# Kernel optimization log

Measured on AMD Instinct MI355X. Metric: run time of the kernel, lower is better.

The kernel has to match this reference:

```python
import jax, jax.numpy as jnp
import numpy as np
from jax.scipy.special import i0

# torchkbnufft default configuration
N = 256          # image size per dim (im_size)
OSF = 2          # grid oversampling factor (default grid_size = 2*im_size)
G = N * OSF      # oversampled grid size = 512
W = 6            # kernel width (numpoints default)
ALPHA = 2.34 * W # Kaiser-Bessel shape parameter (kbwidth default 2.34)
M = 65536        # number of non-uniform k-space samples
B, C = 2, 8      # batch, coils


def _kb_ft(t):
    """Analytic Fourier transform of the KB kernel (for deapodization)."""
    s2 = ALPHA ** 2 - (jnp.pi * W * t) ** 2
    z = jnp.sqrt(jnp.abs(s2)) + 1e-12
    return jnp.where(s2 >= 0, jnp.sinh(z) / z, jnp.sin(z) / z)


def _kb(d):
    """Kaiser-Bessel interpolation kernel, d = distance in grid units."""
    u = 1.0 - (2.0 * d / W) ** 2
    return jnp.where(u > 0, i0(ALPHA * jnp.sqrt(jnp.maximum(u, 1e-12))), 0.0) / W


def setup_inputs() -> dict:
    key = jax.random.key(0)
    k1, k2 = jax.random.split(key)
    x_image = jax.random.normal(k1, (B, C, N, N), dtype=jnp.float32)
    # trajectory in radians/sample, uniform in [-pi, pi)
    k_traj = (jax.random.uniform(k2, (2, M), dtype=jnp.float32) - 0.5) * (2 * jnp.pi)
    return {"x_image": x_image, "k_traj": k_traj}


def reference(x_image, k_traj):
    # 1) deapodization (scaling coefficients), centered image convention
    n = jnp.arange(N, dtype=jnp.float32) - N / 2
    sc = 1.0 / _kb_ft(n / G)                       # (N,)
    xs = (x_image * (sc[:, None] * sc[None, :])).astype(jnp.complex64)

    # 2) zero-pad onto oversampled grid with image centered at index 0 (mod G)
    grid = jnp.zeros(x_image.shape[:2] + (G, G), jnp.complex64)
    grid = grid.at[..., :N, :N].set(xs)
    grid = jnp.roll(grid, shift=(-(N // 2), -(N // 2)), axis=(-2, -1))
    Xk = jnp.fft.fft2(grid)                        # (B,C,G,G) uniform k-space

    # 3) KB interpolation onto non-uniform points (irregular gather)
    tm = k_traj * (G / (2 * jnp.pi))               # continuous grid coords, (2,M)
    offs = jnp.arange(-(W // 2) + 1, W // 2 + 1, dtype=jnp.float32)  # [-2..3]
    base = jnp.floor(tm)
    pts = base[:, :, None] + offs                  # (2,M,W) neighbor coords
    wts = _kb(tm[:, :, None] - pts)                # (2,M,W) real weights
    idx = pts.astype(jnp.int32) % G                # wrap (periodic grid)

    gathered = Xk[:, :, idx[0][:, :, None], idx[1][:, None, :]]  # (B,C,M,W,W)
    y = jnp.einsum('bcmij,mi,mj->bcm', gathered,
                   wts[0].astype(jnp.complex64), wts[1].astype(jnp.complex64))
    # return complex result as stacked (real, imag) float32 for the harness
    return jnp.stack([y.real, y.imag], axis=-1)   # (B,C,M,2)
```

## Files before the change

kernel.cpp:

```cpp
#include <hip/hip_runtime.h>
#include <hip/hip_fp16.h>
#include <math.h>

#define NN 256
#define GSZ 512
#define GG (GSZ * GSZ)
#define BC 16
#define MM 65536
#define ALPHA_C 14.04f
#define WKER 6
#define PI_F 3.14159265358979f
#define RC2 0.70710678118654752f
#define KSCALE 81.48733086305042f

#define SSCALE 16777216.0f
#define INV_SSCALE 5.9604644775390625e-8f

#define CAP 160
#define TRW 21
#define TPITCH 23
#define PLANE (TRW * TPITCH)
#define QPL 4
#define NPQ (QPL * TRW * TRW)

__device__ __forceinline__ __half2* gh_plane(float2* grid, int bc) {
    return (__half2*)((char*)grid + (size_t)bc * (GG * 8) + 524288);
}
__device__ __forceinline__ const __half2* gh_plane_c(const float2* grid, int bc) {
    return (const __half2*)((const char*)grid + (size_t)bc * (GG * 8) + 524288);
}


__device__ __forceinline__ float bessel_i0(float x) {
    if (x < 3.75f) {
        float t = x * (1.0f / 3.75f);
        float t2 = t * t;
        return 1.0f + t2 * (3.5156229f + t2 * (3.0899424f + t2 * (1.2067492f +
                     t2 * (0.2659732f + t2 * (0.0360768f + t2 * 0.0045813f)))));
    } else {
        float t = 3.75f / x;
        float p = 0.39894228f + t * (0.01328592f + t * (0.00225319f + t * (-0.00157565f +
                  t * (0.00916281f + t * (-0.02057706f + t * (0.02635537f +
                  t * (-0.01647633f + t * 0.00392377f)))))));
        return p * __expf(x) * rsqrtf(x);
    }
}

__device__ __forceinline__ float kb_weight(float d) {
    float r = d * (2.0f / (float)WKER);
    float u = 1.0f - r * r;
    if (u <= 0.0f) return 0.0f;
    return bessel_i0(ALPHA_C * sqrtf(u)) * (1.0f / (float)WKER);
}

__device__ __forceinline__ float kb_ft_inv(float t) {
    float a = PI_F * (float)WKER * t;
    float s2 = ALPHA_C * ALPHA_C - a * a;
    float z = sqrtf(fabsf(s2)) + 1e-12f;
    float sh = 0.5f * (__expf(z) - __expf(-z));
    return z / sh;
}

__device__ __forceinline__ void cmul(float& zr, float& zi, float wr, float wi) {
    float r = zr * wr - zi * wi;
    zi = zr * wi + zi * wr;
    zr = r;
}


template <int L>
__device__ __forceinline__ void radix8_stage(float* pr, float* pi_, int j) {
    int pos = j & (L - 1);
    int base = (j - pos) * 8 + pos;
    float ar[8], ai[8];
#pragma unroll
    for (int r = 0; r < 8; ++r) {
        int idx = base + r * L;
        int ph = idx + (idx >> 3);
        ar[r] = pr[ph];
        ai[r] = pi_[ph];
    }
    if (L > 1) {
        float th = (float)pos * (-PI_F / (4.0f * (float)L));
        float s1, c1;
        __sincosf(th, &s1, &c1);
        float wr = c1, wi = s1;
#pragma unroll
        for (int r = 1; r < 8; ++r) {
            cmul(ar[r], ai[r], wr, wi);
            float nr = wr * c1 - wi * s1;
            wi = wr * s1 + wi * c1;
            wr = nr;
        }
    }
    float s0r = ar[0] + ar[4], s0i = ai[0] + ai[4];
    float d0r = ar[0] - ar[4], d0i = ai[0] - ai[4];
    float s1r = ar[2] + ar[6], s1i = ai[2] + ai[6];
    float d1r = ar[2] - ar[6], d1i = ai[2] - ai[6];
    float E0r = s0r + s1r, E0i = s0i + s1i;
    float E2r = s0r - s1r, E2i = s0i - s1i;
    float E1r = d0r + d1i, E1i = d0i - d1r;
    float E3r = d0r - d1i, E3i = d0i + d1r;
    float u0r = ar[1] + ar[5], u0i = ai[1] + ai[5];
    float v0r = ar[1] - ar[5], v0i = ai[1] - ai[5];
    float u1r = ar[3] + ar[7], u1i = ai[3] + ai[7];
    float v1r = ar[3] - ar[7], v1i = ai[3] - ai[7];
    float O0r = u0r + u1r, O0i = u0i + u1i;
    float O2r = u0r - u1r, O2i = u0i - u1i;
    float O1r = v0r + v1i, O1i = v0i - v1r;
    float O3r = v0r - v1i, O3i = v0i + v1r;
    float t1r = RC2 * (O1r + O1i), t1i = RC2 * (O1i - O1r);
    float t2r = O2i,               t2i = -O2r;
    float t3r = RC2 * (O3i - O3r), t3i = -RC2 * (O3r + O3i);
    float xr[8], xi[8];
    xr[0] = E0r + O0r; xi[0] = E0i + O0i;
    xr[4] = E0r - O0r; xi[4] = E0i - O0i;
    xr[1] = E1r + t1r; xi[1] = E1i + t1i;
    xr[5] = E1r - t1r; xi[5] = E1i - t1i;
    xr[2] = E2r + t2r; xi[2] = E2i + t2i;
    xr[6] = E2r - t2r; xi[6] = E2i - t2i;
    xr[3] = E3r + t3r; xi[3] = E3i + t3i;
    xr[7] = E3r - t3r; xi[7] = E3i - t3i;
#pragma unroll
    for (int q = 0; q < 8; ++q) {
        int idx = base + q * L;
        int ph = idx + (idx >> 3);
        pr[ph] = xr[q];
        pi_[ph] = xi[q];
    }
}


#define LDSP 576
__global__ void __launch_bounds__(256) k_fft_row(const float* __restrict__ x,
                                                 float2* __restrict__ grid) {
    __shared__ float re[4][LDSP], im[4][LDSP];
    int b = blockIdx.x;
    int t = threadIdx.x;
    int w = t >> 6;
    int l = t & 63;
    int rg = (b & 63) * 4 + w;
    int bc = b >> 6;
    int r = (rg < 128) ? rg : rg + 256;
    int r_img = rg ^ 128;
    float scx = kb_ft_inv((float)(r_img - 128) * (1.0f / (float)GSZ));
    const float* xrow = x + ((size_t)bc * NN + (size_t)r_img) * NN;
#pragma unroll
    for (int e = 0; e < 8; ++e) {
        int i = e * 64 + l;
        float v = 0.0f;
        if (i < 128 || i >= 384) {
            int y = (i + 128) & (GSZ - 1);
            float scy = kb_ft_inv((float)(y - 128) * (1.0f / (float)GSZ));
            v = xrow[y] * scx * scy;
        }
        int rev = (l & 7) * 64 + (l >> 3) * 8 + e;
        int ph = rev + (rev >> 3);
        re[w][ph] = v;
        im[w][ph] = 0.0f;
    }
    __syncthreads();
    radix8_stage<1>(re[w], im[w], l);
    __syncthreads();
    radix8_stage<8>(re[w], im[w], l);
    __syncthreads();
    radix8_stage<64>(re[w], im[w], l);
    __syncthreads();
    size_t gbase = (size_t)bc * GG + (size_t)r * GSZ;
#pragma unroll
    for (int e = 0; e < 8; ++e) {
        int k = e * 64 + l;
        int ph = k + (k >> 3);
        grid[gbase + k] = make_float2(re[w][ph], im[w][ph]);
    }
}

#define CSTR 577
__global__ void __launch_bounds__(256) k_fft_col(float2* __restrict__ grid) {
    __shared__ float re[16][CSTR], im[16][CSTR];
    int b = blockIdx.x;
    int bc = b >> 5;
    int c0 = (b & 31) << 4;
    size_t base = (size_t)bc * GG + (size_t)c0;
    int t = threadIdx.x;
#pragma unroll
    for (int it = 0; it < 32; ++it) {
        int idx = it * 256 + t;
        int row = idx >> 4, col = idx & 15;
        float2 v = make_float2(0.0f, 0.0f);
        if (row < 128 || row >= 384)
            v = grid[base + (size_t)row * GSZ + col];
        int rev = (row & 7) * 64 + ((row >> 3) & 7) * 8 + (row >> 6);
        int ph = rev + (rev >> 3);
        re[col][ph] = v.x;
        im[col][ph] = v.y;
    }
    __syncthreads();
    int col = t & 15, jg = t >> 4;
#pragma unroll
    for (int k = 0; k < 4; ++k) radix8_stage<1>(re[col], im[col], jg + 16 * k);
    __syncthreads();
#pragma unroll
    for (int k = 0; k < 4; ++k) radix8_stage<8>(re[col], im[col], jg + 16 * k);
    __syncthreads();
#pragma unroll
    for (int k = 0; k < 4; ++k) radix8_stage<64>(re[col], im[col], jg + 16 * k);
    __syncthreads();
    __half2* ghp = gh_plane(grid, bc);
#pragma unroll
    for (int it = 0; it < 32; ++it) {
        int idx = it * 256 + t;
        int row = idx >> 4, c = idx & 15;
        int ph = row + (row >> 3);
        ghp[(size_t)row * GSZ + c0 + c] = __float22half2_rn(
            make_float2(re[c][ph] * SSCALE, im[c][ph] * SSCALE));
    }
}


__global__ void k_bin(const float* __restrict__ kt, unsigned* __restrict__ cnt,
                      unsigned short* __restrict__ ubuf) {
    int m = blockIdx.x * blockDim.x + threadIdx.x;
    float tmx = kt[m] * KSCALE;
    float tmy = kt[MM + m] * KSCALE;
    int ibx = (int)floorf(tmx) & (GSZ - 1);
    int iby = (int)floorf(tmy) & (GSZ - 1);
    int tile = ((ibx >> 4) << 5) | (iby >> 4);
    unsigned slot = atomicAdd(&cnt[tile], 1u);
    if (slot < CAP) ubuf[(size_t)tile * CAP + slot] = (unsigned short)m;
}


__global__ void __launch_bounds__(128) k_gather_tile(
    const float2* __restrict__ grid, const float* __restrict__ kt,
    const unsigned* __restrict__ cnt, const unsigned short* __restrict__ ubuf,
    float2* __restrict__ out) {
    __shared__ __half2 ldsh[QPL * PLANE];
    __shared__ float wts[CAP][13];
    __shared__ unsigned lxy[CAP];
    int bid = blockIdx.x;
    int b = ((bid & 7) << 9) | (bid >> 3);
    int tile = b >> 2;
    int quad = b & 3;
    int bc0 = quad * QPL;
    int tx0 = (tile >> 5) << 4;
    int ty0 = (tile & 31) << 4;
    int t = threadIdx.x;
#pragma unroll
    for (int k = 0; k < 14; ++k) {
        int idx = t + (k << 7);
        if (idx < NPQ) {
            int p = idx / (TRW * TRW);
            int rem = idx - p * (TRW * TRW);
            int r = rem / TRW;
            int c = rem - r * TRW;
            int row = (tx0 - 2 + r) & (GSZ - 1);
            int col = (ty0 - 2 + c) & (GSZ - 1);
            ldsh[p * PLANE + r * TPITCH + c] =
                gh_plane_c(grid, bc0 + p)[(size_t)row * GSZ + col];
        }
    }
    int n = (int)cnt[tile];
    if (n > CAP) n = CAP;
    for (int p = t; p < n; p += 128) {
        int m = (int)ubuf[(size_t)tile * CAP + p];
        float tmx = kt[m] * KSCALE;
        float tmy = kt[MM + m] * KSCALE;
        float bx = floorf(tmx), by = floorf(tmy);
#pragma unroll
        for (int o = 0; o < 6; ++o) {
            float offv = (float)(o - 2);
            wts[p][o]     = kb_weight(tmx - (bx + offv)) * INV_SSCALE;
            wts[p][6 + o] = kb_weight(tmy - (by + offv));
        }
        int lx = (int)bx & 15;
        int ly = (int)by & 15;
        lxy[p] = ((unsigned)m << 8) | (unsigned)(lx << 4) | (unsigned)ly;
    }
    __syncthreads();
    int g = t >> 6;
    int baseA = (2 * g) * PLANE;
    int baseB = baseA + PLANE;
    int bcA = bc0 + 2 * g, bcB = bcA + 1;
    for (int s = (t & 63); s < n; s += 64) {
        unsigned lc = lxy[s];
        int m = (int)(lc >> 8);
        int lx = (int)((lc >> 4) & 15u);
        int ly = (int)(lc & 15u);
        float w0v[6], w1v[6];
#pragma unroll
        for (int o = 0; o < 6; ++o) {
            w0v[o] = wts[s][o];
            w1v[o] = wts[s][6 + o];
        }
        int off0 = lx * TPITCH + ly;
        float arA = 0.f, aiA = 0.f, arB = 0.f, aiB = 0.f;
#pragma unroll
        for (int ii = 0; ii < 6; ++ii) {
            float wi = w0v[ii];
            int rowoff = off0 + ii * TPITCH;
#pragma unroll
            for (int j = 0; j < 6; ++j) {
                float wv = wi * w1v[j];
                int o = rowoff + j;
                float2 vA = __half22float2(ldsh[baseA + o]);
                float2 vB = __half22float2(ldsh[baseB + o]);
                arA = fmaf(wv, vA.x, arA);
                aiA = fmaf(wv, vA.y, aiA);
                arB = fmaf(wv, vB.x, arB);
                aiB = fmaf(wv, vB.y, aiB);
            }
        }
        out[(size_t)bcA * MM + m] = make_float2(arA, aiA);
        out[(size_t)bcB * MM + m] = make_float2(arB, aiB);
    }
}

__global__ void k_gather(const float2* __restrict__ grid, const float* __restrict__ kt,
                         float2* __restrict__ out) {
    int tid = blockIdx.x * blockDim.x + threadIdx.x;
    int m = tid & (MM - 1);
    int bc = tid >> 16;
    float tmx = kt[m] * KSCALE;
    float tmy = kt[MM + m] * KSCALE;
    float bx = floorf(tmx), by = floorf(tmy);
    int ibx = (int)bx, iby = (int)by;
    float w0[6], w1[6];
    int ix[6], iy[6];
#pragma unroll
    for (int o = 0; o < 6; ++o) {
        float offv = (float)(o - 2);
        w0[o] = kb_weight(tmx - (bx + offv)) * INV_SSCALE;
        w1[o] = kb_weight(tmy - (by + offv));
        ix[o] = (ibx + (o - 2) + GSZ) & (GSZ - 1);
        iy[o] = (iby + (o - 2) + GSZ) & (GSZ - 1);
    }
    const __half2* img = gh_plane_c(grid, bc);
    float ar = 0.0f, ai = 0.0f;
#pragma unroll
    for (int i = 0; i < 6; ++i) {
        const __half2* rowp = img + (size_t)ix[i] * GSZ;
        float wi = w0[i];
#pragma unroll
        for (int j = 0; j < 6; ++j) {
            float2 v = __half22float2(rowp[iy[j]]);
            float wv = wi * w1[j];
            ar = fmaf(wv, v.x, ar);
            ai = fmaf(wv, v.y, ai);
        }
    }
    out[(size_t)bc * MM + m] = make_float2(ar, ai);
}


extern "C" void kernel_launch(void* const* d_in, const int* in_sizes, int n_in,
                              void* d_out, int out_size, void* d_ws, size_t ws_size,
                              hipStream_t stream) {
    const float* x = (const float*)d_in[0];
    const float* kt = (const float*)d_in[1];
    float2* out = (float2*)d_out;
    char* ws = (char*)d_ws;

    const size_t GRID_BYTES = (size_t)BC * GG * sizeof(float2);
    const size_t CNT_BYTES = 1024 * sizeof(unsigned);
    const size_t UBUF_BYTES = (size_t)1024 * CAP * sizeof(unsigned short);
    float2* grid = (float2*)ws;
    unsigned* cnt = (unsigned*)(ws + GRID_BYTES);
    unsigned short* ubuf = (unsigned short*)(ws + GRID_BYTES + CNT_BYTES);
    const size_t NEED = GRID_BYTES + CNT_BYTES + UBUF_BYTES;

    if (ws_size >= NEED) {
        hipMemsetAsync(cnt, 0, CNT_BYTES, stream);
        k_bin<<<MM / 256, 256, 0, stream>>>(kt, cnt, ubuf);
        k_fft_row<<<BC * 64, 256, 0, stream>>>(x, grid);
        k_fft_col<<<BC * (GSZ / 16), 256, 0, stream>>>(grid);
        k_gather_tile<<<4096, 128, 0, stream>>>(grid, kt, cnt, ubuf, out);
    } else {
        k_fft_row<<<BC * 64, 256, 0, stream>>>(x, grid);
        k_fft_col<<<BC * (GSZ / 16), 256, 0, stream>>>(grid);
        k_gather<<<(BC * MM) / 256, 256, 0, stream>>>(grid, kt, out);
    }
}
```

Before: 77.50 us.

## Fuse binning into row FFT launch and compute KB weights inline in gather

After: 75.91 us. 1.02x faster.

```diff
diff --git a/kernel.cpp b/kernel.cpp
--- a/kernel.cpp
+++ b/kernel.cpp
@@ -132,6 +132,214 @@
 
 
 #define LDSP 576
+#define ROWBLK (BC * 64)
+__global__ void __launch_bounds__(256) k_fft_row_bin(
+    const float* __restrict__ x, float2* __restrict__ grid,
+    const float* __restrict__ kt, unsigned* __restrict__ cnt,
+    unsigned short* __restrict__ ubuf) {
+    __shared__ float re[4][LDSP], im[4][LDSP];
+    int b = blockIdx.x;
+    int t = threadIdx.x;
+    if (b >= ROWBLK) {
+        int m = (b - ROWBLK) * 256 + t;
+        float tmx = kt[m] * KSCALE;
+        float tmy = kt[MM + m] * KSCALE;
+        int ibx = (int)floorf(tmx) & (GSZ - 1);
+        int iby = (int)floorf(tmy) & (GSZ - 1);
+        int tile = ((ibx >> 4) << 5) | (iby >> 4);
+        unsigned slot = atomicAdd(&cnt[tile], 1u);
+        if (slot < CAP) ubuf[(size_t)tile * CAP + slot] = (unsigned short)m;
+        return;
+    }
+    int w = t >> 6;
+    int l = t & 63;
+    int rg = (b & 63) * 4 + w;
+    int bc = b >> 6;
+    int r = (rg < 128) ? rg : rg + 256;
+    int r_img = rg ^ 128;
+    float scx = kb_ft_inv((float)(r_img - 128) * (1.0f / (float)GSZ));
+    const float* xrow = x + ((size_t)bc * NN + (size_t)r_img) * NN;
+#pragma unroll
+    for (int e = 0; e < 8; ++e) {
+        int i = e * 64 + l;
+        float v = 0.0f;
+        if (i < 128 || i >= 384) {
+            int y = (i + 128) & (GSZ - 1);
+            float scy = kb_ft_inv((float)(y - 128) * (1.0f / (float)GSZ));
+            v = xrow[y] * scx * scy;
+        }
+        int rev = (l & 7) * 64 + (l >> 3) * 8 + e;
+        int ph = rev + (rev >> 3);
+        re[w][ph] = v;
+        im[w][ph] = 0.0f;
+    }
+    __syncthreads();
+    radix8_stage<1>(re[w], im[w], l);
+    __syncthreads();
+    radix8_stage<8>(re[w], im[w], l);
+    __syncthreads();
+    radix8_stage<64>(re[w], im[w], l);
+    __syncthreads();
+    size_t gbase = (size_t)bc * GG + (size_t)r * GSZ;
+#pragma unroll
+    for (int e = 0; e < 8; ++e) {
+        int k = e * 64 + l;
+        int ph = k + (k >> 3);
+        grid[gbase + k] = make_float2(re[w][ph], im[w][ph]);
+    }
+}
+
+
+#define CSTR 577
+__global__ void __launch_bounds__(256) k_fft_col(float2* __restrict__ grid) {
+    __shared__ float re[16][CSTR], im[16][CSTR];
+    int b = blockIdx.x;
+    int bc = b >> 5;
+    int c0 = (b & 31) << 4;
+    size_t base = (size_t)bc * GG + (size_t)c0;
+    int t = threadIdx.x;
+#pragma unroll
+    for (int it = 0; it < 32; ++it) {
+        int idx = it * 256 + t;
+        int row = idx >> 4, col = idx & 15;
+        float2 v = make_float2(0.0f, 0.0f);
+        if (row < 128 || row >= 384)
+            v = grid[base + (size_t)row * GSZ + col];
+        int rev = (row & 7) * 64 + ((row >> 3) & 7) * 8 + (row >> 6);
+        int ph = rev + (rev >> 3);
+        re[col][ph] = v.x;
+        im[col][ph] = v.y;
+    }
+    __syncthreads();
+    int col = t & 15, jg = t >> 4;
+#pragma unroll
+    for (int k = 0; k < 4; ++k) radix8_stage<1>(re[col], im[col], jg + 16 * k);
+    __syncthreads();
+#pragma unroll
+    for (int k = 0; k < 4; ++k) radix8_stage<8>(re[col], im[col], jg + 16 * k);
+    __syncthreads();
+#pragma unroll
+    for (int k = 0; k < 4; ++k) radix8_stage<64>(re[col], im[col], jg + 16 * k);
+    __syncthreads();
+    __half2* ghp = gh_plane(grid, bc);
+#pragma unroll
+    for (int it = 0; it < 32; ++it) {
+        int idx = it * 256 + t;
+        int row = idx >> 4, c = idx & 15;
+        int ph = row + (row >> 3);
+        ghp[(size_t)row * GSZ + c0 + c] = __float22half2_rn(
+            make_float2(re[c][ph] * SSCALE, im[c][ph] * SSCALE));
+    }
+}
+
+
+__global__ void __launch_bounds__(128, 6) k_gather_tile(
+    const float2* __restrict__ grid, const float* __restrict__ kt,
+    const unsigned* __restrict__ cnt, const unsigned short* __restrict__ ubuf,
+    float2* __restrict__ out) {
+    __shared__ __half2 ldsh[QPL * PLANE];
+    int bid = blockIdx.x;
+    int b = ((bid & 7) << 9) | (bid >> 3);
+    int tile = b >> 2;
+    int quad = b & 3;
+    int bc0 = quad * QPL;
+    int tx0 = (tile >> 5) << 4;
+    int ty0 = (tile & 31) << 4;
+    int t = threadIdx.x;
+#pragma unroll
+    for (int k = 0; k < 14; ++k) {
+        int idx = t + (k << 7);
+        if (idx < NPQ) {
+            int p = idx / (TRW * TRW);
+            int rem = idx - p * (TRW * TRW);
+            int r = rem / TRW;
+            int c = rem - r * TRW;
+            int row = (tx0 - 2 + r) & (GSZ - 1);
+            int col = (ty0 - 2 + c) & (GSZ - 1);
+            ldsh[p * PLANE + r * TPITCH + c] =
+                gh_plane_c(grid, bc0 + p)[(size_t)row * GSZ + col];
+        }
+    }
+    int n = (int)cnt[tile];
+    if (n > CAP) n = CAP;
+    __syncthreads();
+    int g = t >> 6;
+    int baseA = (2 * g) * PLANE;
+    int baseB = baseA + PLANE;
+    int bcA = bc0 + 2 * g, bcB = bcA + 1;
+    for (int s = (t & 63); s < n; s += 64) {
+        int m = (int)ubuf[(size_t)tile * CAP + s];
+        float tmx = kt[m] * KSCALE;
+        float tmy = kt[MM + m] * KSCALE;
+        float bx = floorf(tmx), by = floorf(tmy);
+        float w0v[6], w1v[6];
+#pragma unroll
+        for (int o = 0; o < 6; ++o) {
+            float offv = (float)(o - 2);
+            w0v[o] = kb_weight(tmx - (bx + offv)) * INV_SSCALE;
+            w1v[o] = kb_weight(tmy - (by + offv));
+        }
+        int lx = (int)bx & 15;
+        int ly = (int)by & 15;
+        int off0 = lx * TPITCH + ly;
+        float arA = 0.f, aiA = 0.f, arB = 0.f, aiB = 0.f;
+#pragma unroll
+        for (int ii = 0; ii < 6; ++ii) {
+            float wi = w0v[ii];
+            int rowoff = off0 + ii * TPITCH;
+#pragma unroll
+            for (int j = 0; j < 6; ++j) {
+                float wv = wi * w1v[j];
+                int o = rowoff + j;
+                float2 vA = __half22float2(ldsh[baseA + o]);
+                float2 vB = __half22float2(ldsh[baseB + o]);
+                arA = fmaf(wv, vA.x, arA);
+                aiA = fmaf(wv, vA.y, aiA);
+                arB = fmaf(wv, vB.x, arB);
+                aiB = fmaf(wv, vB.y, aiB);
+            }
+        }
+        out[(size_t)bcA * MM + m] = make_float2(arA, aiA);
+        out[(size_t)bcB * MM + m] = make_float2(arB, aiB);
+    }
+}
+
+__global__ void k_gather(const float2* __restrict__ grid, const float* __restrict__ kt,
+                         float2* __restrict__ out) {
+    int tid = blockIdx.x * blockDim.x + threadIdx.x;
+    int m = tid & (MM - 1);
+    int bc = tid >> 16;
+    float tmx = kt[m] * KSCALE;
+    float tmy = kt[MM + m] * KSCALE;
+    float bx = floorf(tmx), by = floorf(tmy);
+    int ibx = (int)bx, iby = (int)by;
+    float w0[6], w1[6];
+    int ix[6], iy[6];
+#pragma unroll
+    for (int o = 0; o < 6; ++o) {
+        float offv = (float)(o - 2);
+        w0[o] = kb_weight(tmx - (bx + offv)) * INV_SSCALE;
+        w1[o] = kb_weight(tmy - (by + offv));
+        ix[o] = (ibx + (o - 2) + GSZ) & (GSZ - 1);
+        iy[o] = (iby + (o - 2) + GSZ) & (GSZ - 1);
+    }
+    const __half2* img = gh_plane_c(grid, bc);
+    float ar = 0.0f, ai = 0.0f;
+#pragma unroll
+    for (int i = 0; i < 6; ++i) {
+        const __half2* rowp = img + (size_t)ix[i] * GSZ;
+        float wi = w0[i];
+#pragma unroll
+        for (int j = 0; j < 6; ++j) {
+            float2 v = __half22float2(rowp[iy[j]]);
+            float wv = wi * w1[j];
+            ar = fmaf(wv, v.x, ar);
+            ai = fmaf(wv, v.y, ai);
+        }
+    }
+    out[(size_t)bc * MM + m] = make_float2(ar, ai);
+}
+
 __global__ void __launch_bounds__(256) k_fft_row(const float* __restrict__ x,
                                                  float2* __restrict__ grid) {
     __shared__ float re[4][LDSP], im[4][LDSP];
@@ -175,183 +383,6 @@
     }
 }
 
-#define CSTR 577
-__global__ void __launch_bounds__(256) k_fft_col(float2* __restrict__ grid) {
-    __shared__ float re[16][CSTR], im[16][CSTR];
-    int b = blockIdx.x;
-    int bc = b >> 5;
-    int c0 = (b & 31) << 4;
-    size_t base = (size_t)bc * GG + (size_t)c0;
-    int t = threadIdx.x;
-#pragma unroll
-    for (int it = 0; it < 32; ++it) {
-        int idx = it * 256 + t;
-        int row = idx >> 4, col = idx & 15;
-        float2 v = make_float2(0.0f, 0.0f);
-        if (row < 128 || row >= 384)
-            v = grid[base + (size_t)row * GSZ + col];
-        int rev = (row & 7) * 64 + ((row >> 3) & 7) * 8 + (row >> 6);
-        int ph = rev + (rev >> 3);
-        re[col][ph] = v.x;
-        im[col][ph] = v.y;
-    }
-    __syncthreads();
-    int col = t & 15, jg = t >> 4;
-#pragma unroll
-    for (int k = 0; k < 4; ++k) radix8_stage<1>(re[col], im[col], jg + 16 * k);
-    __syncthreads();
-#pragma unroll
-    for (int k = 0; k < 4; ++k) radix8_stage<8>(re[col], im[col], jg + 16 * k);
-    __syncthreads();
-#pragma unroll
-    for (int k = 0; k < 4; ++k) radix8_stage<64>(re[col], im[col], jg + 16 * k);
-    __syncthreads();
-    __half2* ghp = gh_plane(grid, bc);
-#pragma unroll
-    for (int it = 0; it < 32; ++it) {
-        int idx = it * 256 + t;
-        int row = idx >> 4, c = idx & 15;
-        int ph = row + (row >> 3);
-        ghp[(size_t)row * GSZ + c0 + c] = __float22half2_rn(
-            make_float2(re[c][ph] * SSCALE, im[c][ph] * SSCALE));
-    }
-}
-
-
-__global__ void k_bin(const float* __restrict__ kt, unsigned* __restrict__ cnt,
-                      unsigned short* __restrict__ ubuf) {
-    int m = blockIdx.x * blockDim.x + threadIdx.x;
-    float tmx = kt[m] * KSCALE;
-    float tmy = kt[MM + m] * KSCALE;
-    int ibx = (int)floorf(tmx) & (GSZ - 1);
-    int iby = (int)floorf(tmy) & (GSZ - 1);
-    int tile = ((ibx >> 4) << 5) | (iby >> 4);
-    unsigned slot = atomicAdd(&cnt[tile], 1u);
-    if (slot < CAP) ubuf[(size_t)tile * CAP + slot] = (unsigned short)m;
-}
-
-
-__global__ void __launch_bounds__(128) k_gather_tile(
-    const float2* __restrict__ grid, const float* __restrict__ kt,
-    const unsigned* __restrict__ cnt, const unsigned short* __restrict__ ubuf,
-    float2* __restrict__ out) {
-    __shared__ __half2 ldsh[QPL * PLANE];
-    __shared__ float wts[CAP][13];
-    __shared__ unsigned lxy[CAP];
-    int bid = blockIdx.x;
-    int b = ((bid & 7) << 9) | (bid >> 3);
-    int tile = b >> 2;
-    int quad = b & 3;
-    int bc0 = quad * QPL;
-    int tx0 = (tile >> 5) << 4;
-    int ty0 = (tile & 31) << 4;
-    int t = threadIdx.x;
-#pragma unroll
-    for (int k = 0; k < 14; ++k) {
-        int idx = t + (k << 7);
-        if (idx < NPQ) {
-            int p = idx / (TRW * TRW);
-            int rem = idx - p * (TRW * TRW);
-            int r = rem / TRW;
-            int c = rem - r * TRW;
-            int row = (tx0 - 2 + r) & (GSZ - 1);
-            int col = (ty0 - 2 + c) & (GSZ - 1);
-            ldsh[p * PLANE + r * TPITCH + c] =
-                gh_plane_c(grid, bc0 + p)[(size_t)row * GSZ + col];
-        }
-    }
-    int n = (int)cnt[tile];
-    if (n > CAP) n = CAP;
-    for (int p = t; p < n; p += 128) {
-        int m = (int)ubuf[(size_t)tile * CAP + p];
-        float tmx = kt[m] * KSCALE;
-        float tmy = kt[MM + m] * KSCALE;
-        float bx = floorf(tmx), by = floorf(tmy);
-#pragma unroll
-        for (int o = 0; o < 6; ++o) {
-            float offv = (float)(o - 2);
-            wts[p][o]     = kb_weight(tmx - (bx + offv)) * INV_SSCALE;
-            wts[p][6 + o] = kb_weight(tmy - (by + offv));
-        }
-        int lx = (int)bx & 15;
-        int ly = (int)by & 15;
-        lxy[p] = ((unsigned)m << 8) | (unsigned)(lx << 4) | (unsigned)ly;
-    }
-    __syncthreads();
-    int g = t >> 6;
-    int baseA = (2 * g) * PLANE;
-    int baseB = baseA + PLANE;
-    int bcA = bc0 + 2 * g, bcB = bcA + 1;
-    for (int s = (t & 63); s < n; s += 64) {
-        unsigned lc = lxy[s];
-        int m = (int)(lc >> 8);
-        int lx = (int)((lc >> 4) & 15u);
-        int ly = (int)(lc & 15u);
-        float w0v[6], w1v[6];
-#pragma unroll
-        for (int o = 0; o < 6; ++o) {
-            w0v[o] = wts[s][o];
-            w1v[o] = wts[s][6 + o];
-        }
-        int off0 = lx * TPITCH + ly;
-        float arA = 0.f, aiA = 0.f, arB = 0.f, aiB = 0.f;
-#pragma unroll
-        for (int ii = 0; ii < 6; ++ii) {
-            float wi = w0v[ii];
-            int rowoff = off0 + ii * TPITCH;
-#pragma unroll
-            for (int j = 0; j < 6; ++j) {
-                float wv = wi * w1v[j];
-                int o = rowoff + j;
-                float2 vA = __half22float2(ldsh[baseA + o]);
-                float2 vB = __half22float2(ldsh[baseB + o]);
-                arA = fmaf(wv, vA.x, arA);
-                aiA = fmaf(wv, vA.y, aiA);
-                arB = fmaf(wv, vB.x, arB);
-                aiB = fmaf(wv, vB.y, aiB);
-            }
-        }
-        out[(size_t)bcA * MM + m] = make_float2(arA, aiA);
-        out[(size_t)bcB * MM + m] = make_float2(arB, aiB);
-    }
-}
-
-__global__ void k_gather(const float2* __restrict__ grid, const float* __restrict__ kt,
-                         float2* __restrict__ out) {
-    int tid = blockIdx.x * blockDim.x + threadIdx.x;
-    int m = tid & (MM - 1);
-    int bc = tid >> 16;
-    float tmx = kt[m] * KSCALE;
-    float tmy = kt[MM + m] * KSCALE;
-    float bx = floorf(tmx), by = floorf(tmy);
-    int ibx = (int)bx, iby = (int)by;
-    float w0[6], w1[6];
-    int ix[6], iy[6];
-#pragma unroll
-    for (int o = 0; o < 6; ++o) {
-        float offv = (float)(o - 2);
-        w0[o] = kb_weight(tmx - (bx + offv)) * INV_SSCALE;
-        w1[o] = kb_weight(tmy - (by + offv));
-        ix[o] = (ibx + (o - 2) + GSZ) & (GSZ - 1);
-        iy[o] = (iby + (o - 2) + GSZ) & (GSZ - 1);
-    }
-    const __half2* img = gh_plane_c(grid, bc);
-    float ar = 0.0f, ai = 0.0f;
-#pragma unroll
-    for (int i = 0; i < 6; ++i) {
-        const __half2* rowp = img + (size_t)ix[i] * GSZ;
-        float wi = w0[i];
-#pragma unroll
-        for (int j = 0; j < 6; ++j) {
-            float2 v = __half22float2(rowp[iy[j]]);
-            float wv = wi * w1[j];
-            ar = fmaf(wv, v.x, ar);
-            ai = fmaf(wv, v.y, ai);
-        }
-    }
-    out[(size_t)bc * MM + m] = make_float2(ar, ai);
-}
-
 
 extern "C" void kernel_launch(void* const* d_in, const int* in_sizes, int n_in,
                               void* d_out, int out_size, void* d_ws, size_t ws_size,
@@ -371,8 +402,7 @@
 
     if (ws_size >= NEED) {
         hipMemsetAsync(cnt, 0, CNT_BYTES, stream);
-        k_bin<<<MM / 256, 256, 0, stream>>>(kt, cnt, ubuf);
-        k_fft_row<<<BC * 64, 256, 0, stream>>>(x, grid);
+        k_fft_row_bin<<<ROWBLK + 256, 256, 0, stream>>>(x, grid, kt, cnt, ubuf);
         k_fft_col<<<BC * (GSZ / 16), 256, 0, stream>>>(grid);
         k_gather_tile<<<4096, 128, 0, stream>>>(grid, kt, cnt, ubuf, out);
     } else {
```
